# Kernel tuning notes

Hardware: AMD Instinct MI355X
Metric: run time of the kernel (lower is better)

The kernel has to match this reference:

```python
import jax, jax.numpy as jnp
import numpy as np

B, LQ, LKV, D, H = 4, 1024, 4096, 512, 4
HD = D // H  # head dim = 128


def setup_inputs() -> dict:
    key = jax.random.key(0)
    ks = jax.random.split(key, 6)
    s = 1.0 / np.sqrt(D)
    return {
        "x": jax.random.normal(ks[0], (B, LQ, D), jnp.float32),
        "encoder_feats": jax.random.normal(ks[1], (B, LKV, D), jnp.float32),
        "Wq": jax.random.normal(ks[2], (D, D), jnp.float32) * s,
        "Wk": jax.random.normal(ks[3], (D, D), jnp.float32) * s,
        "Wv": jax.random.normal(ks[4], (D, D), jnp.float32) * s,
        "bq": jnp.zeros((D,), jnp.float32),
        "bk": jnp.zeros((D,), jnp.float32),
        "bv": jnp.zeros((D,), jnp.float32),
        "Wo": jax.random.normal(ks[5], (D, D), jnp.float32) * s,
        "bo": jnp.zeros((D,), jnp.float32),
    }


def reference(x, encoder_feats, Wq, Wk, Wv, bq, bk, bv, Wo, bo):
    # nn.MultiheadAttention explicit (non-flash) path, dropout=0, eval.
    # Project, split heads: [B, L, D] -> [B, H, L, HD]
    def heads(t, L):
        return t.reshape(B, L, H, HD).transpose(0, 2, 1, 3)

    q = heads(x @ Wq.T + bq, LQ)
    k = heads(encoder_feats @ Wk.T + bk, LKV)
    v = heads(encoder_feats @ Wv.T + bv, LKV)

    scale = 1.0 / jnp.sqrt(jnp.asarray(HD, x.dtype))
    scores = jnp.einsum("bhqd,bhkd->bhqk", q, k) * scale  # [B,H,LQ,LKV]
    attn = jax.nn.softmax(scores, axis=-1)
    ctx = jnp.einsum("bhqk,bhkd->bhqd", attn, v)  # [B,H,LQ,HD]
    ctx = ctx.transpose(0, 2, 1, 3).reshape(B, LQ, D)
    attn_output = ctx @ Wo.T + bo
    # forward() returns attn_output only (fused/LayerNorm result is discarded)
    return attn_output
```

## Files before the change

### kernel.cpp

```cpp
#include <hip/hip_runtime.h>
#include <math.h>

#define B_    4
#define LQ_   1024
#define LKV_  4096
#define DM    512
#define NH    4
#define HD_   128

typedef _Float16 half8   __attribute__((ext_vector_type(8)));
typedef _Float16 half4_t __attribute__((ext_vector_type(4)));
typedef float    floatx4 __attribute__((ext_vector_type(4)));

#define MFMA16(a, b, c) __builtin_amdgcn_mfma_f32_16x16x32_f16((a), (b), (c), 0, 0, 0)

__global__ __launch_bounds__(256) void prep_w(
    const float* __restrict__ Wq, const float* __restrict__ Wk,
    const float* __restrict__ Wv, const float* __restrict__ Wo,
    _Float16* __restrict__ Wh)
{
  int i = blockIdx.x * 256 + threadIdx.x;
  int wsel = i >> 16;
  const float* src = (wsel == 0) ? Wq : (wsel == 1) ? Wk : (wsel == 2) ? Wv : Wo;
  size_t off = i & 65535;
  float4 v = *(const float4*)(src + off * 4);
  half4_t h;
  h[0] = (_Float16)v.x; h[1] = (_Float16)v.y;
  h[2] = (_Float16)v.z; h[3] = (_Float16)v.w;
  *(half4_t*)(Wh + ((size_t)wsel << 18) + off * 4) = h;
}

__global__ __launch_bounds__(256, 2) void proj_qkv(
    const float* __restrict__ x,
    const float* __restrict__ enc,
    const _Float16* __restrict__ Whq,
    const _Float16* __restrict__ Whk,
    const _Float16* __restrict__ Whv,
    const float* __restrict__ bq,
    const float* __restrict__ bk,
    const float* __restrict__ bv,
    _Float16* __restrict__ Qh,
    _Float16* __restrict__ Kh,
    _Float16* __restrict__ Vt,
    float qscale)
{
  __shared__ _Float16 SM[3 * 128 * 72];
  _Float16 (*Xs)[72]  = (_Float16(*)[72])SM;
  _Float16 (*Ws1)[72] = (_Float16(*)[72])(SM + 128 * 72);
  _Float16 (*Ws2)[72] = (_Float16(*)[72])(SM + 2 * 128 * 72);

  const int tid  = threadIdx.x;
  const int lane = tid & 63;
  const int w    = tid >> 6;
  const int n16  = lane & 15;
  const int quad = lane >> 4;
  const int wm   = (w & 1) * 64;
  const int wn   = (w >> 1) * 64;
  const int col0 = blockIdx.y * 128;

  if ((int)blockIdx.x >= 128) {
    const int row0 = ((int)blockIdx.x - 128) * 128;
    floatx4 acc[4][4];
#pragma unroll
    for (int a = 0; a < 4; ++a)
#pragma unroll
      for (int b = 0; b < 4; ++b) acc[a][b] = (floatx4){0.f, 0.f, 0.f, 0.f};

    for (int k0 = 0; k0 < 512; k0 += 64) {
#pragma unroll
      for (int i = 0; i < 4; ++i) {
        int c = i * 256 + tid;
        int r = c >> 3, off = (c & 7) * 8;
        const float* xp = x + (size_t)(row0 + r) * 512 + k0 + off;
        float4 a = *(const float4*)xp, b2 = *(const float4*)(xp + 4);
        half8 hx;
        hx[0] = (_Float16)a.x;  hx[1] = (_Float16)a.y;
        hx[2] = (_Float16)a.z;  hx[3] = (_Float16)a.w;
        hx[4] = (_Float16)b2.x; hx[5] = (_Float16)b2.y;
        hx[6] = (_Float16)b2.z; hx[7] = (_Float16)b2.w;
        *(half8*)&Xs[r][off] = hx;
        *(half8*)&Ws1[r][off] = *(const half8*)(Whq + (size_t)(col0 + r) * 512 + k0 + off);
      }
      __syncthreads();
#pragma unroll
      for (int kc = 0; kc < 2; ++kc) {
        half8 af[4], bf[4];
#pragma unroll
        for (int mb = 0; mb < 4; ++mb)
          af[mb] = *(const half8*)&Xs[wm + mb * 16 + n16][kc * 32 + quad * 8];
#pragma unroll
        for (int nb = 0; nb < 4; ++nb)
          bf[nb] = *(const half8*)&Ws1[wn + nb * 16 + n16][kc * 32 + quad * 8];
#pragma unroll
        for (int mb = 0; mb < 4; ++mb)
#pragma unroll
          for (int nb = 0; nb < 4; ++nb)
            acc[mb][nb] = MFMA16(af[mb], bf[nb], acc[mb][nb]);
      }
      __syncthreads();
    }
#pragma unroll
    for (int mb = 0; mb < 4; ++mb)
#pragma unroll
      for (int nb = 0; nb < 4; ++nb)
#pragma unroll
        for (int r = 0; r < 4; ++r) {
          int row = row0 + wm + mb * 16 + quad * 4 + r;
          int col = col0 + wn + nb * 16 + n16;
          Qh[(size_t)row * 512 + col] =
              (_Float16)((acc[mb][nb][r] + bq[col]) * qscale);
        }
    return;
  }

  const int row0 = (int)blockIdx.x * 128;
  floatx4 accK[4][4], accV[4][4];
#pragma unroll
  for (int a = 0; a < 4; ++a)
#pragma unroll
    for (int b = 0; b < 4; ++b) {
      accK[a][b] = (floatx4){0.f, 0.f, 0.f, 0.f};
      accV[a][b] = (floatx4){0.f, 0.f, 0.f, 0.f};
    }

  for (int k0 = 0; k0 < 512; k0 += 64) {
#pragma unroll
    for (int i = 0; i < 4; ++i) {
      int c = i * 256 + tid;
      int r = c >> 3, off = (c & 7) * 8;
      const float* xp = enc + (size_t)(row0 + r) * 512 + k0 + off;
      float4 a = *(const float4*)xp, b2 = *(const float4*)(xp + 4);
      half8 hx;
      hx[0] = (_Float16)a.x;  hx[1] = (_Float16)a.y;
      hx[2] = (_Float16)a.z;  hx[3] = (_Float16)a.w;
      hx[4] = (_Float16)b2.x; hx[5] = (_Float16)b2.y;
      hx[6] = (_Float16)b2.z; hx[7] = (_Float16)b2.w;
      *(half8*)&Xs[r][off] = hx;
      *(half8*)&Ws1[r][off] = *(const half8*)(Whk + (size_t)(col0 + r) * 512 + k0 + off);
      *(half8*)&Ws2[r][off] = *(const half8*)(Whv + (size_t)(col0 + r) * 512 + k0 + off);
    }
    __syncthreads();
#pragma unroll
    for (int kc = 0; kc < 2; ++kc) {
      half8 af[4], bkf[4], bvf[4];
#pragma unroll
      for (int mb = 0; mb < 4; ++mb)
        af[mb] = *(const half8*)&Xs[wm + mb * 16 + n16][kc * 32 + quad * 8];
#pragma unroll
      for (int nb = 0; nb < 4; ++nb) {
        bkf[nb] = *(const half8*)&Ws1[wn + nb * 16 + n16][kc * 32 + quad * 8];
        bvf[nb] = *(const half8*)&Ws2[wn + nb * 16 + n16][kc * 32 + quad * 8];
      }
#pragma unroll
      for (int mb = 0; mb < 4; ++mb)
#pragma unroll
        for (int nb = 0; nb < 4; ++nb) {
          accK[mb][nb] = MFMA16(af[mb], bkf[nb], accK[mb][nb]);
          accV[mb][nb] = MFMA16(af[mb], bvf[nb], accV[mb][nb]);
        }
    }
    __syncthreads();
  }

#pragma unroll
  for (int mb = 0; mb < 4; ++mb)
#pragma unroll
    for (int nb = 0; nb < 4; ++nb)
#pragma unroll
      for (int r = 0; r < 4; ++r) {
        int row = row0 + wm + mb * 16 + quad * 4 + r;
        int col = col0 + wn + nb * 16 + n16;
        Kh[(size_t)row * 512 + col] = (_Float16)(accK[mb][nb][r] + bk[col]);
      }

  _Float16 (*Ts)[144] = (_Float16(*)[144])SM;
#pragma unroll
  for (int mb = 0; mb < 4; ++mb)
#pragma unroll
    for (int nb = 0; nb < 4; ++nb) {
      int dl = wn + nb * 16 + n16;
      float bi = bv[col0 + dl];
      half4_t hv;
#pragma unroll
      for (int r = 0; r < 4; ++r) hv[r] = (_Float16)(accV[mb][nb][r] + bi);
      *(half4_t*)&Ts[dl][wm + mb * 16 + quad * 4] = hv;
    }
  __syncthreads();
  int b   = row0 >> 12;
  int kv0 = row0 & 4095;
#pragma unroll
  for (int i = 0; i < 8; ++i) {
    int f = i * 256 + tid;
    int dl = f >> 4, kv8 = (f & 15) * 8;
    half8 ov = *(const half8*)&Ts[dl][kv8];
    *(half8*)(Vt + (size_t)((b * 4 + blockIdx.y) * 128 + dl) * LKV_ + kv0 + kv8) = ov;
  }
}

__global__ __launch_bounds__(256, 2) void flash_mfma2(
    const _Float16* __restrict__ Qh,
    const _Float16* __restrict__ Kh,
    const _Float16* __restrict__ Vtg,
    _Float16* __restrict__ Opart,
    float* __restrict__ ml)
{
  __shared__ _Float16 U[4 * 32 * 72];
  __shared__ _Float16 Vs[128][72];
  _Float16 (*Ks)[136] = (_Float16(*)[136])U;
  _Float16* Ps = U;

  const int tid  = threadIdx.x;
  const int lane = tid & 63;
  const int w    = tid >> 6;
  const int n16  = lane & 15;
  const int quad = lane >> 4;

  const int xb    = blockIdx.x;
  const int qt    = blockIdx.y;
  const int split = xb & 3;
  const int bh    = xb >> 2;
  const int h = bh & 3, b = bh >> 2;

  const _Float16* Qg = Qh + (size_t)(b * LQ_ + qt * 128) * DM + h * HD_;
  const _Float16* Kg = Kh + (size_t)(b * LKV_) * DM + h * HD_;
  const _Float16* Vg = Vtg + (size_t)(bh * HD_) * LKV_;

  half8 qf[2][4];
  const int chunk = w >> 1;
  const int qrb   = (w & 1) * 32;
#pragma unroll
  for (int c = 0; c < 2; ++c) {
#pragma unroll
    for (int i = 0; i < 4; ++i) {
      int f = i * 256 + tid;
      int r = f >> 4, c8 = (f & 15) * 8;
      *(half8*)&Ks[r][c8] = *(const half8*)(Qg + (size_t)(c * 64 + r) * DM + c8);
    }
    __syncthreads();
    if (chunk == c) {
#pragma unroll
      for (int qb = 0; qb < 2; ++qb)
#pragma unroll
        for (int kc = 0; kc < 4; ++kc)
          qf[qb][kc] = *(const half8*)&Ks[qrb + qb * 16 + n16][kc * 32 + quad * 8];
    }
    __syncthreads();
  }

  floatx4 o[2][8];
#pragma unroll
  for (int mb = 0; mb < 2; ++mb)
#pragma unroll
    for (int vb = 0; vb < 8; ++vb) o[mb][vb] = (floatx4){0.f, 0.f, 0.f, 0.f};
  float m_i[2] = {-INFINITY, -INFINITY};
  float l_i[2] = {0.f, 0.f};

  for (int kt = split * 16; kt < split * 16 + 16; ++kt) {
#pragma unroll
    for (int i = 0; i < 4; ++i) {
      int f = i * 256 + tid;
      int r = f >> 4, c8 = (f & 15) * 8;
      *(half8*)&Ks[r][c8] = *(const half8*)(Kg + (size_t)(kt * 64 + r) * DM + c8);
    }
#pragma unroll
    for (int i = 0; i < 4; ++i) {
      int f = i * 256 + tid;
      int d = f >> 3, kv8 = (f & 7) * 8;
      *(half8*)&Vs[d][kv8] = *(const half8*)(Vg + (size_t)d * LKV_ + kt * 64 + kv8);
    }
    __syncthreads();

    floatx4 s[2][4];
#pragma unroll
    for (int qb = 0; qb < 2; ++qb)
#pragma unroll
      for (int cb = 0; cb < 4; ++cb) s[qb][cb] = (floatx4){0.f, 0.f, 0.f, 0.f};
#pragma unroll
    for (int cb = 0; cb < 4; ++cb) {
#pragma unroll
      for (int kc = 0; kc < 4; ++kc) {
        half8 kf = *(const half8*)&Ks[cb * 16 + n16][kc * 32 + quad * 8];
        s[0][cb] = MFMA16(kf, qf[0][kc], s[0][cb]);
        s[1][cb] = MFMA16(kf, qf[1][kc], s[1][cb]);
      }
    }
    __syncthreads();

    float alpha[2];
#pragma unroll
    for (int qb = 0; qb < 2; ++qb) {
      float mx = -INFINITY;
#pragma unroll
      for (int cb = 0; cb < 4; ++cb)
#pragma unroll
        for (int r = 0; r < 4; ++r) mx = fmaxf(mx, s[qb][cb][r]);
      mx = fmaxf(mx, __shfl_xor(mx, 16));
      mx = fmaxf(mx, __shfl_xor(mx, 32));
      float mn = fmaxf(m_i[qb], mx);
      alpha[qb] = __expf(m_i[qb] - mn);
      m_i[qb] = mn;
      float rs = 0.f;
#pragma unroll
      for (int cb = 0; cb < 4; ++cb) {
        half4_t ph;
#pragma unroll
        for (int r = 0; r < 4; ++r) {
          float p = __expf(s[qb][cb][r] - mn);
          rs += p;
          ph[r] = (_Float16)p;
        }
        *(half4_t*)&Ps[(w * 32 + qb * 16 + n16) * 72 + cb * 16 + quad * 4] = ph;
      }
      rs += __shfl_xor(rs, 16);
      rs += __shfl_xor(rs, 32);
      l_i[qb] = l_i[qb] * alpha[qb] + rs;
    }

    if (__ballot((alpha[0] != 1.f) || (alpha[1] != 1.f))) {
#pragma unroll
      for (int mb = 0; mb < 2; ++mb) {
#pragma unroll
        for (int r = 0; r < 4; ++r) {
          float a = __shfl(alpha[mb], (lane & 48) | (quad * 4 + r));
#pragma unroll
          for (int vb = 0; vb < 8; ++vb) o[mb][vb][r] *= a;
        }
      }
    }

    half8 pf[2][2];
#pragma unroll
    for (int mb = 0; mb < 2; ++mb)
#pragma unroll
      for (int kc = 0; kc < 2; ++kc)
        pf[mb][kc] = *(const half8*)&Ps[(w * 32 + mb * 16 + n16) * 72 + kc * 32 + quad * 8];
#pragma unroll
    for (int vb = 0; vb < 8; ++vb) {
#pragma unroll
      for (int kc = 0; kc < 2; ++kc) {
        half8 vf = *(const half8*)&Vs[vb * 16 + n16][kc * 32 + quad * 8];
        o[0][vb] = MFMA16(pf[0][kc], vf, o[0][vb]);
        o[1][vb] = MFMA16(pf[1][kc], vf, o[1][vb]);
      }
    }
    __syncthreads();
  }

  _Float16* Og = Opart + ((size_t)xb * 1024 + qt * 128 + w * 32) * HD_;
#pragma unroll
  for (int mb = 0; mb < 2; ++mb)
#pragma unroll
    for (int r = 0; r < 4; ++r)
#pragma unroll
      for (int vb = 0; vb < 8; ++vb)
        Og[(size_t)(mb * 16 + quad * 4 + r) * HD_ + vb * 16 + n16] =
            (_Float16)o[mb][vb][r];
  if (quad == 0) {
#pragma unroll
    for (int qb = 0; qb < 2; ++qb) {
      size_t qi = (size_t)xb * 1024 + qt * 128 + w * 32 + qb * 16 + n16;
      ml[qi * 2] = m_i[qb];
      ml[qi * 2 + 1] = l_i[qb];
    }
  }
}

__global__ __launch_bounds__(256) void combine_splits(
    const _Float16* __restrict__ Opart,
    const float* __restrict__ ml,
    _Float16* __restrict__ CTXh)
{
  int g  = blockIdx.x * 2 + (threadIdx.x >> 7);
  int d  = threadIdx.x & 127;
  int bh = g >> 10, q = g & 1023;
  int b = bh >> 2, h = bh & 3;

  float m[4], l[4], M = -INFINITY;
#pragma unroll
  for (int p = 0; p < 4; ++p) {
    size_t idx = ((size_t)(bh * 4 + p) * 1024 + q) * 2;
    m[p] = ml[idx]; l[p] = ml[idx + 1];
    M = fmaxf(M, m[p]);
  }
  float L = 0.f, o = 0.f;
#pragma unroll
  for (int p = 0; p < 4; ++p) {
    float wgt = __expf(m[p] - M);
    L += wgt * l[p];
    o += wgt * (float)Opart[((size_t)(bh * 4 + p) * 1024 + q) * HD_ + d];
  }
  CTXh[(size_t)(b * LQ_ + q) * DM + h * HD_ + d] = (_Float16)(o / L);
}

__global__ __launch_bounds__(256) void proj_out(
    const _Float16* __restrict__ X,
    const _Float16* __restrict__ W,
    const float* __restrict__ bias,
    float* __restrict__ Y)
{
  __shared__ _Float16 Xs[128][72];
  __shared__ _Float16 Ws[128][72];

  const int tid  = threadIdx.x;
  const int lane = tid & 63;
  const int w    = tid >> 6;
  const int n16  = lane & 15;
  const int quad = lane >> 4;
  const int wm   = (w & 1) * 64;
  const int wn   = (w >> 1) * 64;
  const int row0 = blockIdx.x * 128;
  const int col0 = blockIdx.y * 128;

  floatx4 acc[4][4];
#pragma unroll
  for (int a = 0; a < 4; ++a)
#pragma unroll
    for (int b = 0; b < 4; ++b) acc[a][b] = (floatx4){0.f, 0.f, 0.f, 0.f};

  for (int k0 = 0; k0 < 512; k0 += 64) {
#pragma unroll
    for (int i = 0; i < 4; ++i) {
      int c = i * 256 + tid;
      int r = c >> 3, off = (c & 7) * 8;
      *(half8*)&Xs[r][off] = *(const half8*)(X + (size_t)(row0 + r) * 512 + k0 + off);
      *(half8*)&Ws[r][off] = *(const half8*)(W + (size_t)(col0 + r) * 512 + k0 + off);
    }
    __syncthreads();
#pragma unroll
    for (int kc = 0; kc < 2; ++kc) {
      half8 af[4], bf[4];
#pragma unroll
      for (int mb = 0; mb < 4; ++mb)
        af[mb] = *(const half8*)&Xs[wm + mb * 16 + n16][kc * 32 + quad * 8];
#pragma unroll
      for (int nb = 0; nb < 4; ++nb)
        bf[nb] = *(const half8*)&Ws[wn + nb * 16 + n16][kc * 32 + quad * 8];
#pragma unroll
      for (int mb = 0; mb < 4; ++mb)
#pragma unroll
        for (int nb = 0; nb < 4; ++nb)
          acc[mb][nb] = MFMA16(af[mb], bf[nb], acc[mb][nb]);
    }
    __syncthreads();
  }

#pragma unroll
  for (int mb = 0; mb < 4; ++mb)
#pragma unroll
    for (int nb = 0; nb < 4; ++nb)
#pragma unroll
      for (int r = 0; r < 4; ++r) {
        int row = row0 + wm + mb * 16 + quad * 4 + r;
        int col = col0 + wn + nb * 16 + n16;
        Y[(size_t)row * 512 + col] = acc[mb][nb][r] + bias[col];
      }
}

extern "C" void kernel_launch(void* const* d_in, const int* in_sizes, int n_in,
                              void* d_out, int out_size, void* d_ws, size_t ws_size,
                              hipStream_t stream) {
  const float* x   = (const float*)d_in[0];
  const float* enc = (const float*)d_in[1];
  const float* Wq  = (const float*)d_in[2];
  const float* Wk  = (const float*)d_in[3];
  const float* Wv  = (const float*)d_in[4];
  const float* bq  = (const float*)d_in[5];
  const float* bk  = (const float*)d_in[6];
  const float* bv  = (const float*)d_in[7];
  const float* Wo  = (const float*)d_in[8];
  const float* bo  = (const float*)d_in[9];
  float* out = (float*)d_out;

  char* ws = (char*)d_ws;
  _Float16* Qh    = (_Float16*)(ws);
  _Float16* Kh    = (_Float16*)(ws + (4u  << 20));
  _Float16* Vtg   = (_Float16*)(ws + (20u << 20));
  _Float16* Opart = (_Float16*)(ws + (36u << 20));
  _Float16* CTXh  = (_Float16*)(ws + (52u << 20));
  float*    mlp   = (float*)   (ws + (56u << 20));
  _Float16* Wh    = (_Float16*)(ws + (57u << 20));

  _Float16* Whq = Wh;
  _Float16* Whk = Wh + 262144;
  _Float16* Whv = Wh + 524288;
  _Float16* Who = Wh + 786432;

  const float qscale = 0.08838834764831845f;
  dim3 blk(256);

  prep_w<<<dim3(1024), blk, 0, stream>>>(Wq, Wk, Wv, Wo, Wh);

  proj_qkv<<<dim3(160, 4), blk, 0, stream>>>(
      x, enc, Whq, Whk, Whv, bq, bk, bv, Qh, Kh, Vtg, qscale);

  flash_mfma2<<<dim3(64, 8), blk, 0, stream>>>(Qh, Kh, Vtg, Opart, mlp);

  combine_splits<<<dim3(8192), blk, 0, stream>>>(Opart, mlp, CTXh);

  proj_out<<<dim3(32, 4), blk, 0, stream>>>(CTXh, Who, bo, out);
}
```

Before: 202.3 us.

## Swizzle flash-attention LDS tiles and fuse split combine into output projection

Replaces padded LDS arrays in the flash kernel with XOR-swizzled unpadded layouts for K, V, Q staging and P, to avoid bank conflicts while reducing LDS footprint. Removes the separate combine_splits kernel and CTX buffer by computing per-row split weights inside the output projection kernel and combining the four partial outputs while loading the A tile. The output projection now uses 64-row tiles with twice as many blocks, so each block's partial outputs are re-read for every column block (4x redundant combine reads).

```diff
diff --git a/kernel.cpp b/kernel.cpp
--- a/kernel.cpp
+++ b/kernel.cpp
@@ -13,6 +13,8 @@
 typedef float    floatx4 __attribute__((ext_vector_type(4)));
 
 #define MFMA16(a, b, c) __builtin_amdgcn_mfma_f32_16x16x32_f16((a), (b), (c), 0, 0, 0)
+
+#define SWZ(c, r) ((c) ^ (((r) & 7) << 3))
 
 __global__ __launch_bounds__(256) void prep_w(
     const float* __restrict__ Wq, const float* __restrict__ Wk,
@@ -204,9 +206,9 @@
     _Float16* __restrict__ Opart,
     float* __restrict__ ml)
 {
-  __shared__ _Float16 U[4 * 32 * 72];
-  __shared__ _Float16 Vs[128][72];
-  _Float16 (*Ks)[136] = (_Float16(*)[136])U;
+  __shared__ _Float16 U[64 * 128];
+  __shared__ _Float16 Vs[128 * 64];
+  _Float16* Ks = U;
   _Float16* Ps = U;
 
   const int tid  = threadIdx.x;
@@ -234,15 +236,18 @@
     for (int i = 0; i < 4; ++i) {
       int f = i * 256 + tid;
       int r = f >> 4, c8 = (f & 15) * 8;
-      *(half8*)&Ks[r][c8] = *(const half8*)(Qg + (size_t)(c * 64 + r) * DM + c8);
+      *(half8*)&Ks[r * 128 + SWZ(c8, r)] =
+          *(const half8*)(Qg + (size_t)(c * 64 + r) * DM + c8);
     }
     __syncthreads();
     if (chunk == c) {
 #pragma unroll
-      for (int qb = 0; qb < 2; ++qb)
+      for (int qb = 0; qb < 2; ++qb) {
+        int qr = qrb + qb * 16 + n16;
 #pragma unroll
         for (int kc = 0; kc < 4; ++kc)
-          qf[qb][kc] = *(const half8*)&Ks[qrb + qb * 16 + n16][kc * 32 + quad * 8];
+          qf[qb][kc] = *(const half8*)&Ks[qr * 128 + SWZ(kc * 32 + quad * 8, qr)];
+      }
     }
     __syncthreads();
   }
@@ -260,13 +265,15 @@
     for (int i = 0; i < 4; ++i) {
       int f = i * 256 + tid;
       int r = f >> 4, c8 = (f & 15) * 8;
-      *(half8*)&Ks[r][c8] = *(const half8*)(Kg + (size_t)(kt * 64 + r) * DM + c8);
+      *(half8*)&Ks[r * 128 + SWZ(c8, r)] =
+          *(const half8*)(Kg + (size_t)(kt * 64 + r) * DM + c8);
     }
 #pragma unroll
     for (int i = 0; i < 4; ++i) {
       int f = i * 256 + tid;
       int d = f >> 3, kv8 = (f & 7) * 8;
-      *(half8*)&Vs[d][kv8] = *(const half8*)(Vg + (size_t)d * LKV_ + kt * 64 + kv8);
+      *(half8*)&Vs[d * 64 + SWZ(kv8, d)] =
+          *(const half8*)(Vg + (size_t)d * LKV_ + kt * 64 + kv8);
     }
     __syncthreads();
 
@@ -277,9 +284,10 @@
       for (int cb = 0; cb < 4; ++cb) s[qb][cb] = (floatx4){0.f, 0.f, 0.f, 0.f};
 #pragma unroll
     for (int cb = 0; cb < 4; ++cb) {
+      int kr = cb * 16 + n16;
 #pragma unroll
       for (int kc = 0; kc < 4; ++kc) {
-        half8 kf = *(const half8*)&Ks[cb * 16 + n16][kc * 32 + quad * 8];
+        half8 kf = *(const half8*)&Ks[kr * 128 + SWZ(kc * 32 + quad * 8, kr)];
         s[0][cb] = MFMA16(kf, qf[0][kc], s[0][cb]);
         s[1][cb] = MFMA16(kf, qf[1][kc], s[1][cb]);
       }
@@ -300,6 +308,7 @@
       alpha[qb] = __expf(m_i[qb] - mn);
       m_i[qb] = mn;
       float rs = 0.f;
+      int pr = w * 32 + qb * 16 + n16;
 #pragma unroll
       for (int cb = 0; cb < 4; ++cb) {
         half4_t ph;
@@ -309,7 +318,7 @@
           rs += p;
           ph[r] = (_Float16)p;
         }
-        *(half4_t*)&Ps[(w * 32 + qb * 16 + n16) * 72 + cb * 16 + quad * 4] = ph;
+        *(half4_t*)&Ps[pr * 64 + SWZ(cb * 16 + quad * 4, pr)] = ph;
       }
       rs += __shfl_xor(rs, 16);
       rs += __shfl_xor(rs, 32);
@@ -330,15 +339,18 @@
 
     half8 pf[2][2];
 #pragma unroll
-    for (int mb = 0; mb < 2; ++mb)
+    for (int mb = 0; mb < 2; ++mb) {
+      int pr = w * 32 + mb * 16 + n16;
 #pragma unroll
       for (int kc = 0; kc < 2; ++kc)
-        pf[mb][kc] = *(const half8*)&Ps[(w * 32 + mb * 16 + n16) * 72 + kc * 32 + quad * 8];
+        pf[mb][kc] = *(const half8*)&Ps[pr * 64 + SWZ(kc * 32 + quad * 8, pr)];
+    }
 #pragma unroll
     for (int vb = 0; vb < 8; ++vb) {
+      int vr = vb * 16 + n16;
 #pragma unroll
       for (int kc = 0; kc < 2; ++kc) {
-        half8 vf = *(const half8*)&Vs[vb * 16 + n16][kc * 32 + quad * 8];
+        half8 vf = *(const half8*)&Vs[vr * 64 + SWZ(kc * 32 + quad * 8, vr)];
         o[0][vb] = MFMA16(pf[0][kc], vf, o[0][vb]);
         o[1][vb] = MFMA16(pf[1][kc], vf, o[1][vb]);
       }
@@ -365,78 +377,95 @@
   }
 }
 
-__global__ __launch_bounds__(256) void combine_splits(
+__global__ __launch_bounds__(256) void proj_out_fused(
     const _Float16* __restrict__ Opart,
     const float* __restrict__ ml,
-    _Float16* __restrict__ CTXh)
-{
-  int g  = blockIdx.x * 2 + (threadIdx.x >> 7);
-  int d  = threadIdx.x & 127;
-  int bh = g >> 10, q = g & 1023;
-  int b = bh >> 2, h = bh & 3;
-
-  float m[4], l[4], M = -INFINITY;
-#pragma unroll
-  for (int p = 0; p < 4; ++p) {
-    size_t idx = ((size_t)(bh * 4 + p) * 1024 + q) * 2;
-    m[p] = ml[idx]; l[p] = ml[idx + 1];
-    M = fmaxf(M, m[p]);
-  }
-  float L = 0.f, o = 0.f;
-#pragma unroll
-  for (int p = 0; p < 4; ++p) {
-    float wgt = __expf(m[p] - M);
-    L += wgt * l[p];
-    o += wgt * (float)Opart[((size_t)(bh * 4 + p) * 1024 + q) * HD_ + d];
-  }
-  CTXh[(size_t)(b * LQ_ + q) * DM + h * HD_ + d] = (_Float16)(o / L);
-}
-
-__global__ __launch_bounds__(256) void proj_out(
-    const _Float16* __restrict__ X,
-    const _Float16* __restrict__ W,
-    const float* __restrict__ bias,
+    const _Float16* __restrict__ Who,
+    const float* __restrict__ bo,
     float* __restrict__ Y)
 {
-  __shared__ _Float16 Xs[128][72];
+  __shared__ _Float16 Xs[64][72];
   __shared__ _Float16 Ws[128][72];
+  __shared__ float CW[4][64][8];
 
   const int tid  = threadIdx.x;
   const int lane = tid & 63;
   const int w    = tid >> 6;
   const int n16  = lane & 15;
   const int quad = lane >> 4;
-  const int wm   = (w & 1) * 64;
+  const int wm   = (w & 1) * 32;
   const int wn   = (w >> 1) * 64;
-  const int row0 = blockIdx.x * 128;
+  const int row0 = blockIdx.x * 64;
   const int col0 = blockIdx.y * 128;
-
-  floatx4 acc[4][4];
-#pragma unroll
-  for (int a = 0; a < 4; ++a)
-#pragma unroll
-    for (int b = 0; b < 4; ++b) acc[a][b] = (floatx4){0.f, 0.f, 0.f, 0.f};
+  const int b    = row0 >> 10;
+
+  {
+    int h = tid >> 6, r = tid & 63;
+    int q = (row0 + r) & 1023;
+    int bh = b * 4 + h;
+    float m[4], l[4], M = -INFINITY;
+#pragma unroll
+    for (int p = 0; p < 4; ++p) {
+      size_t idx = ((size_t)(bh * 4 + p) * 1024 + q) * 2;
+      m[p] = ml[idx]; l[p] = ml[idx + 1];
+      M = fmaxf(M, m[p]);
+    }
+    float L = 0.f, wts[4];
+#pragma unroll
+    for (int p = 0; p < 4; ++p) { wts[p] = __expf(m[p] - M); L += wts[p] * l[p]; }
+    float inv = 1.f / L;
+#pragma unroll
+    for (int p = 0; p < 4; ++p) CW[h][r][p] = wts[p] * inv;
+    CW[h][r][4] = 0.f;
+  }
+  __syncthreads();
+
+  floatx4 acc[2][4];
+#pragma unroll
+  for (int a = 0; a < 2; ++a)
+#pragma unroll
+    for (int c = 0; c < 4; ++c) acc[a][c] = (floatx4){0.f, 0.f, 0.f, 0.f};
 
   for (int k0 = 0; k0 < 512; k0 += 64) {
+    int h = k0 >> 7, d0 = k0 & 127;
+    int bh = b * 4 + h;
+#pragma unroll
+    for (int i = 0; i < 2; ++i) {
+      int f = i * 256 + tid;
+      int r = f >> 3, c8 = (f & 7) * 8;
+      int q = (row0 + r) & 1023;
+      float w0 = CW[h][r][0], w1 = CW[h][r][1];
+      float w2 = CW[h][r][2], w3 = CW[h][r][3];
+      size_t base = ((size_t)(bh * 4) * 1024 + q) * 128 + d0 + c8;
+      half8 v0 = *(const half8*)(Opart + base);
+      half8 v1 = *(const half8*)(Opart + base + 131072);
+      half8 v2 = *(const half8*)(Opart + base + 262144);
+      half8 v3 = *(const half8*)(Opart + base + 393216);
+      half8 hx;
+#pragma unroll
+      for (int j = 0; j < 8; ++j)
+        hx[j] = (_Float16)(w0 * (float)v0[j] + w1 * (float)v1[j] +
+                           w2 * (float)v2[j] + w3 * (float)v3[j]);
+      *(half8*)&Xs[r][c8] = hx;
+    }
 #pragma unroll
     for (int i = 0; i < 4; ++i) {
-      int c = i * 256 + tid;
-      int r = c >> 3, off = (c & 7) * 8;
-      *(half8*)&Xs[r][off] = *(const half8*)(X + (size_t)(row0 + r) * 512 + k0 + off);
-      *(half8*)&Ws[r][off] = *(const half8*)(W + (size_t)(col0 + r) * 512 + k0 + off);
+      int f = i * 256 + tid;
+      int r = f >> 3, c8 = (f & 7) * 8;
+      *(half8*)&Ws[r][c8] = *(const half8*)(Who + (size_t)(col0 + r) * 512 + k0 + c8);
     }
     __syncthreads();
 #pragma unroll
     for (int kc = 0; kc < 2; ++kc) {
-      half8 af[4], bf[4];
-#pragma unroll
-      for (int mb = 0; mb < 4; ++mb)
+      half8 af[2], bf[4];
+#pragma unroll
+      for (int mb = 0; mb < 2; ++mb)
         af[mb] = *(const half8*)&Xs[wm + mb * 16 + n16][kc * 32 + quad * 8];
 #pragma unroll
       for (int nb = 0; nb < 4; ++nb)
         bf[nb] = *(const half8*)&Ws[wn + nb * 16 + n16][kc * 32 + quad * 8];
 #pragma unroll
-      for (int mb = 0; mb < 4; ++mb)
+      for (int mb = 0; mb < 2; ++mb)
 #pragma unroll
         for (int nb = 0; nb < 4; ++nb)
           acc[mb][nb] = MFMA16(af[mb], bf[nb], acc[mb][nb]);
@@ -445,14 +474,14 @@
   }
 
 #pragma unroll
-  for (int mb = 0; mb < 4; ++mb)
+  for (int mb = 0; mb < 2; ++mb)
 #pragma unroll
     for (int nb = 0; nb < 4; ++nb)
 #pragma unroll
       for (int r = 0; r < 4; ++r) {
         int row = row0 + wm + mb * 16 + quad * 4 + r;
         int col = col0 + wn + nb * 16 + n16;
-        Y[(size_t)row * 512 + col] = acc[mb][nb][r] + bias[col];
+        Y[(size_t)row * 512 + col] = acc[mb][nb][r] + bo[col];
       }
 }
 
@@ -476,9 +505,8 @@
   _Float16* Kh    = (_Float16*)(ws + (4u  << 20));
   _Float16* Vtg   = (_Float16*)(ws + (20u << 20));
   _Float16* Opart = (_Float16*)(ws + (36u << 20));
-  _Float16* CTXh  = (_Float16*)(ws + (52u << 20));
-  float*    mlp   = (float*)   (ws + (56u << 20));
-  _Float16* Wh    = (_Float16*)(ws + (57u << 20));
+  float*    mlp   = (float*)   (ws + (52u << 20));
+  _Float16* Wh    = (_Float16*)(ws + (53u << 20));
 
   _Float16* Whq = Wh;
   _Float16* Whk = Wh + 262144;
@@ -495,7 +523,5 @@
 
   flash_mfma2<<<dim3(64, 8), blk, 0, stream>>>(Qh, Kh, Vtg, Opart, mlp);
 
-  combine_splits<<<dim3(8192), blk, 0, stream>>>(Opart, mlp, CTXh);
-
-  proj_out<<<dim3(32, 4), blk, 0, stream>>>(CTXh, Who, bo, out);
+  proj_out_fused<<<dim3(64, 4), blk, 0, stream>>>(Opart, mlp, Who, bo, out);
 }
```

After: 205.8 us. About the same (+1.7%).
